# Optimization experiments

Hardware: AMD Instinct MI355X
Metric: run time of the kernel (lower is better)

## Reference

```python
import jax, jax.numpy as jnp
import numpy as np

LN_EPS = 1e-5


def setup_inputs() -> dict:
    key = jax.random.key(0)
    ks = jax.random.split(key, 12)
    B, T, U, H, V = 4, 512, 128, 512, 41
    src = jax.random.normal(ks[0], (B, T, H), dtype=jnp.float32)
    tgt = jax.random.normal(ks[1], (B, U, H), dtype=jnp.float32)
    src_len = jax.random.randint(ks[2], (B,), 1, T + 1, dtype=jnp.int32)
    tgt_len = jax.random.randint(ks[3], (B,), 1, U + 1, dtype=jnp.int32)
    s = 1.0 / np.sqrt(H)
    W1 = jax.random.uniform(ks[4], (H, H), jnp.float32, -s, s)
    b1 = jax.random.uniform(ks[5], (H,), jnp.float32, -s, s)
    W2 = jax.random.uniform(ks[6], (H, H), jnp.float32, -s, s)
    b2 = jax.random.uniform(ks[7], (H,), jnp.float32, -s, s)
    ln_g = jnp.ones((H,), jnp.float32)
    ln_b = jnp.zeros((H,), jnp.float32)
    Wl = jax.random.uniform(ks[8], (H, V), jnp.float32, -s, s)
    bl = jax.random.uniform(ks[9], (V,), jnp.float32, -s, s)
    return dict(source_encodings=src, source_lengths=src_len,
                target_encodings=tgt, target_lengths=tgt_len,
                W1=W1, b1=b1, W2=W2, b2=b2, ln_g=ln_g, ln_b=ln_b,
                Wl=Wl, bl=bl)


def _f_target(tgt, W1, b1, W2, b2, ln_g, ln_b):
    h = jax.nn.gelu(tgt @ W1 + b1, approximate=False)  # exact GELU (torch default)
    h = h @ W2 + b2
    mu = jnp.mean(h, axis=-1, keepdims=True)
    var = jnp.var(h, axis=-1, keepdims=True)
    return (h - mu) * jax.lax.rsqrt(var + LN_EPS) * ln_g + ln_b


def reference(source_encodings, source_lengths, target_encodings, target_lengths,
              W1, b1, W2, b2, ln_g, ln_b, Wl, bl):
    tgt = _f_target(target_encodings, W1, b1, W2, b2, ln_g, ln_b)  # [B,U,H]
    # joint broadcast add: [B,T,1,H] + [B,1,U,H] -> [B,T,U,H]
    joint = source_encodings[:, :, None, :] + tgt[:, None, :, :]
    act = jnp.tanh(joint)
    out = act @ Wl + bl  # [B,T,U,V]
    return out, source_lengths, target_lengths
```

## Files before the change

### kernel.cpp

```cpp
#include <hip/hip_runtime.h>
#include <math.h>

#define Bb 4
#define Tt 512
#define Uu 128
#define Hh 512
#define Vv 41

typedef __attribute__((ext_vector_type(8))) short short8;
typedef __attribute__((ext_vector_type(4))) float f32x4;
typedef __attribute__((ext_vector_type(2))) float v2f;

__device__ __forceinline__ unsigned pack_bf16_rne(float hi, float lo) {
    unsigned xh = __float_as_uint(hi); xh += 0x7fffu + ((xh >> 16) & 1u);
    unsigned xl = __float_as_uint(lo); xl += 0x7fffu + ((xl >> 16) & 1u);
    return __builtin_amdgcn_perm(xh, xl, 0x07060302);
}

__device__ __forceinline__ unsigned short bf16_rne(float v) {
    unsigned x = __float_as_uint(v);
    x += 0x7fffu + ((x >> 16) & 1u);
    return (unsigned short)(x >> 16);
}

__device__ __forceinline__ unsigned tanh2_pack(float x0, float x1) {
    v2f xc;
    xc.x = __builtin_amdgcn_fmed3f(x0, -3.0f, 3.0f);
    xc.y = __builtin_amdgcn_fmed3f(x1, -3.0f, 3.0f);
    v2f t = xc * xc;
    v2f p = t * (v2f){-0.00140725f, -0.00140725f} + (v2f){0.0288922f, 0.0288922f};
    p = p * t + (v2f){-0.2177528f, -0.2177528f};
    p = p * t + (v2f){0.9707868f, 0.9707868f};
    v2f g = xc * p;
    return __builtin_amdgcn_perm(__float_as_uint(g.y), __float_as_uint(g.x), 0x07060302);
}

__global__ __launch_bounds__(256) void prep_pack(
    const float* __restrict__ W1, const float* __restrict__ W2,
    const float* __restrict__ Wl, const float* __restrict__ tgt,
    unsigned short* __restrict__ Wp1, unsigned short* __restrict__ Wp2,
    unsigned short* __restrict__ Wpl, unsigned short* __restrict__ tgtA,
    const int* __restrict__ sl, const int* __restrict__ tl,
    float* __restrict__ lenDst)
{
    __shared__ __align__(16) char smem[16640];
    const int bid = blockIdx.x, tid = threadIdx.x;

    if (bid >= 136) {
        unsigned short (*At)[520] = (unsigned short (*)[520])smem;
        const int rt = bid - 136;
        const float4* t4 = (const float4*)(tgt + (size_t)rt * 16 * Hh);
        #pragma unroll
        for (int j = 0; j < 8; ++j) {
            int fi = j * 256 + tid;
            int row = fi >> 7, c4 = fi & 127;
            float4 v = t4[fi];
            uint2 pk;
            pk.x = pack_bf16_rne(v.y, v.x);
            pk.y = pack_bf16_rne(v.w, v.z);
            *(uint2*)&At[row][c4 * 4] = pk;
        }
        __syncthreads();
        #pragma unroll
        for (int i = 0; i < 4; ++i) {
            int chunk = i * 256 + tid;
            int ks = chunk >> 6, l = chunk & 63;
            int q = l >> 4, nc = l & 15;
            short8 v = *(const short8*)&At[nc][ks * 32 + q * 8];
            *(short8*)(tgtA + ((size_t)(rt * 16 + ks) * 64 + l) * 8) = v;
        }
        return;
    }

    if (bid == 135 && tid < 2 * Bb)
        lenDst[tid] = (tid < Bb) ? (float)sl[tid] : (float)tl[tid - Bb];

    float (*T)[65] = (float (*)[65])smem;
    const float* Wsrc; unsigned short* Wdst; int k0, n0, isWl;
    if (bid < 64)       { Wsrc = W1; Wdst = Wp1; k0 = (bid >> 3) * 64; n0 = (bid & 7) * 64; isWl = 0; }
    else if (bid < 128) { Wsrc = W2; Wdst = Wp2; k0 = ((bid - 64) >> 3) * 64; n0 = ((bid - 64) & 7) * 64; isWl = 0; }
    else                { Wsrc = Wl; Wdst = Wpl; k0 = (bid - 128) * 64; n0 = 0; isWl = 1; }

    #pragma unroll
    for (int i = 0; i < 16; ++i) {
        int idx = i * 256 + tid;
        int kk = idx >> 6, nn = idx & 63;
        float v;
        if (isWl) v = (nn < Vv) ? Wl[(k0 + kk) * Vv + nn] : 0.0f;
        else      v = Wsrc[(size_t)(k0 + kk) * 512 + n0 + nn];
        T[kk][nn] = v;
    }
    __syncthreads();

    #pragma unroll
    for (int i = 0; i < 2; ++i) {
        int task = i * 256 + tid;
        int nn = task & 63, kg = task >> 6;
        if (isWl && nn >= 48) continue;
        int n = n0 + nn, k = k0 + kg * 8;
        float e[8];
        #pragma unroll
        for (int j = 0; j < 8; ++j) e[j] = T[kg * 8 + j][nn];
        uint4 pk;
        pk.x = pack_bf16_rne(e[1], e[0]);
        pk.y = pack_bf16_rne(e[3], e[2]);
        pk.z = pack_bf16_rne(e[5], e[4]);
        pk.w = pack_bf16_rne(e[7], e[6]);
        int ntg = n >> 4, ncol = n & 15;
        int ks = (k >> 5) & 15, quad = (k >> 3) & 3;
        int lane = quad * 16 + ncol;
        *(uint4*)(Wdst + (size_t)((ntg * 16 + ks) * 64 + lane) * 8) = pk;
    }
}

__global__ __launch_bounds__(128) void gemm_t1(
    const unsigned short* __restrict__ tgtA,
    const unsigned short* __restrict__ Wp1, const float* __restrict__ b1,
    unsigned short* __restrict__ h1A)
{
    __shared__ unsigned short At[16][72];
    const int nb = blockIdx.x, rt = blockIdx.y;
    const int tid = threadIdx.x, lane = tid & 63, w = tid >> 6;
    const int ncol = lane & 15, quad = lane >> 4;
    const int nt0 = nb * 4 + w * 2;

    const unsigned short* ap = tgtA + ((size_t)rt * 1024 + lane) * 8;
    const unsigned short* bp = Wp1 + (size_t)lane * 8;

    f32x4 acc0 = (f32x4){0.f,0.f,0.f,0.f}, acc1 = (f32x4){0.f,0.f,0.f,0.f};
    short8 ac  = *(const short8*)(ap);
    short8 b0c = *(const short8*)(bp + (size_t)nt0 * 8192);
    short8 b1c = *(const short8*)(bp + (size_t)(nt0 + 1) * 8192);

    #pragma unroll
    for (int ks = 0; ks < 16; ++ks) {
        short8 an, b0n, b1n;
        if (ks < 15) {
            an  = *(const short8*)(ap + (ks + 1) * 512);
            b0n = *(const short8*)(bp + (size_t)nt0 * 8192 + (ks + 1) * 512);
            b1n = *(const short8*)(bp + (size_t)(nt0 + 1) * 8192 + (ks + 1) * 512);
        }
        acc0 = __builtin_amdgcn_mfma_f32_16x16x32_bf16(ac, b0c, acc0, 0, 0, 0);
        acc1 = __builtin_amdgcn_mfma_f32_16x16x32_bf16(ac, b1c, acc1, 0, 0, 0);
        ac = an; b0c = b0n; b1c = b1n;
    }

    #pragma unroll
    for (int nt = 0; nt < 2; ++nt) {
        int n = nb * 64 + w * 32 + nt * 16 + ncol;
        float bias = b1[n];
        f32x4 A = nt ? acc1 : acc0;
        #pragma unroll
        for (int r = 0; r < 4; ++r) {
            float v = A[r] + bias;
            float g = 0.5f * v * (1.0f + erff(v * 0.70710678118654752f));
            At[quad * 4 + r][w * 32 + nt * 16 + ncol] = bf16_rne(g);
        }
    }
    __syncthreads();

    {
        int g2 = w, l = lane;
        short8 v = *(const short8*)&At[l & 15][g2 * 32 + (l >> 4) * 8];
        int ksg = nb * 2 + g2;
        *(short8*)(h1A + ((size_t)(rt * 16 + ksg) * 64 + l) * 8) = v;
    }
}

__global__ __launch_bounds__(128) void gemm_t2(
    const unsigned short* __restrict__ h1A,
    const unsigned short* __restrict__ Wp2, const float* __restrict__ b2,
    float* __restrict__ h2)
{
    const int nb = blockIdx.x, rt = blockIdx.y;
    const int tid = threadIdx.x, lane = tid & 63, w = tid >> 6;
    const int ncol = lane & 15, quad = lane >> 4;
    const int nt0 = nb * 4 + w * 2;

    const unsigned short* ap = h1A + ((size_t)rt * 1024 + lane) * 8;
    const unsigned short* bp = Wp2 + (size_t)lane * 8;

    f32x4 acc0 = (f32x4){0.f,0.f,0.f,0.f}, acc1 = (f32x4){0.f,0.f,0.f,0.f};
    short8 ac  = *(const short8*)(ap);
    short8 b0c = *(const short8*)(bp + (size_t)nt0 * 8192);
    short8 b1c = *(const short8*)(bp + (size_t)(nt0 + 1) * 8192);

    #pragma unroll
    for (int ks = 0; ks < 16; ++ks) {
        short8 an, b0n, b1n;
        if (ks < 15) {
            an  = *(const short8*)(ap + (ks + 1) * 512);
            b0n = *(const short8*)(bp + (size_t)nt0 * 8192 + (ks + 1) * 512);
            b1n = *(const short8*)(bp + (size_t)(nt0 + 1) * 8192 + (ks + 1) * 512);
        }
        acc0 = __builtin_amdgcn_mfma_f32_16x16x32_bf16(ac, b0c, acc0, 0, 0, 0);
        acc1 = __builtin_amdgcn_mfma_f32_16x16x32_bf16(ac, b1c, acc1, 0, 0, 0);
        ac = an; b0c = b0n; b1c = b1n;
    }

    #pragma unroll
    for (int nt = 0; nt < 2; ++nt) {
        int n = nb * 64 + w * 32 + nt * 16 + ncol;
        float bias = b2[n];
        f32x4 A = nt ? acc1 : acc0;
        #pragma unroll
        for (int r = 0; r < 4; ++r)
            h2[(size_t)(rt * 16 + quad * 4 + r) * 512 + n] = A[r] + bias;
    }
}

__global__ __launch_bounds__(256) void ln_kernel(
    const float* __restrict__ h2, const float* __restrict__ ln_g,
    const float* __restrict__ ln_b, float* __restrict__ tgtPf)
{
    const int r = blockIdx.x * 4 + (threadIdx.x >> 6);
    const int lane = threadIdx.x & 63;
    const float4* row4 = (const float4*)(h2 + (size_t)r * Hh);
    float4 v0 = row4[lane], v1 = row4[lane + 64];
    float s = v0.x + v0.y + v0.z + v0.w + v1.x + v1.y + v1.z + v1.w;
    float q = v0.x*v0.x + v0.y*v0.y + v0.z*v0.z + v0.w*v0.w
            + v1.x*v1.x + v1.y*v1.y + v1.z*v1.z + v1.w*v1.w;
    #pragma unroll
    for (int off = 32; off > 0; off >>= 1) {
        s += __shfl_xor(s, off, 64);
        q += __shfl_xor(q, off, 64);
    }
    float mu = s * (1.0f / Hh);
    float rs = rsqrtf(q * (1.0f / Hh) - mu * mu + 1e-5f);

    float4 g0 = ((const float4*)ln_g)[lane], g1 = ((const float4*)ln_g)[lane + 64];
    float4 be0 = ((const float4*)ln_b)[lane], be1 = ((const float4*)ln_b)[lane + 64];
    float4 o0, o1;
    o0.x = (v0.x - mu) * rs * g0.x + be0.x;  o0.y = (v0.y - mu) * rs * g0.y + be0.y;
    o0.z = (v0.z - mu) * rs * g0.z + be0.z;  o0.w = (v0.w - mu) * rs * g0.w + be0.w;
    o1.x = (v1.x - mu) * rs * g1.x + be1.x;  o1.y = (v1.y - mu) * rs * g1.y + be1.y;
    o1.z = (v1.z - mu) * rs * g1.z + be1.z;  o1.w = (v1.w - mu) * rs * g1.w + be1.w;

    const int bb = r >> 7, u = r & 127;
    float* ob = tgtPf + (size_t)bb * 65536 + u * 8;
    int k0 = lane * 4;
    *(float4*)(ob + (k0 >> 3) * 1024 + (k0 & 7)) = o0;
    int k1 = lane * 4 + 256;
    *(float4*)(ob + (k1 >> 3) * 1024 + (k1 & 7)) = o1;
}

__global__ __launch_bounds__(256) void joint_mfma(
    const float* __restrict__ src, const float* __restrict__ tgtPf,
    const unsigned short* __restrict__ Wpl, const float* __restrict__ bl,
    float* __restrict__ out)
{
    __shared__ float srcl[2 * Hh];

    const int t0 = blockIdx.x * 2, b = blockIdx.y, uh = blockIdx.z;
    const int tid = threadIdx.x;
    const int lane = tid & 63, wave = tid >> 6;
    const int ncol = lane & 15, quad = lane >> 4;

    const float4* s4 = (const float4*)(src + ((size_t)(b * Tt + t0)) * Hh);
    ((float4*)srcl)[tid] = s4[tid];

    const int u0 = uh * 64 + (wave & 1) * 32 + ncol;
    const float* pA = tgtPf + (size_t)b * 65536 + u0 * 8;
    const unsigned short* bp = Wpl + (size_t)lane * 8;

    float4 a0 = *(const float4*)(pA + quad * 1024);
    float4 a1 = *(const float4*)(pA + quad * 1024 + 4);
    float4 c0 = *(const float4*)(pA + quad * 1024 + 128);
    float4 c1 = *(const float4*)(pA + quad * 1024 + 132);
    short8 B0 = *(const short8*)(bp);
    short8 B1 = *(const short8*)(bp + 8192);
    short8 B2 = *(const short8*)(bp + 16384);

    f32x4 acc[2][3];
    #pragma unroll
    for (int nt = 0; nt < 3; ++nt) {
        int n = nt * 16 + ncol;
        float bv = (n < Vv) ? bl[n] : 0.0f;
        acc[0][nt] = (f32x4){bv, bv, bv, bv};
        acc[1][nt] = (f32x4){bv, bv, bv, bv};
    }

    __syncthreads();
    const float* srow = srcl + (wave >> 1) * Hh;
    float4 sA = *(const float4*)(srow + quad * 8);
    float4 sB = *(const float4*)(srow + quad * 8 + 4);

    #pragma unroll 4
    for (int ks = 0; ks < 16; ++ks) {
        float4 na0, na1, nc0, nc1, nsA, nsB;
        short8 nB0, nB1, nB2;
        if (ks < 15) {
            const float* pn = pA + ((ks + 1) * 4 + quad) * 1024;
            na0 = *(const float4*)(pn);
            na1 = *(const float4*)(pn + 4);
            nc0 = *(const float4*)(pn + 128);
            nc1 = *(const float4*)(pn + 132);
            nB0 = *(const short8*)(bp + (ks + 1) * 512);
            nB1 = *(const short8*)(bp + 8192 + (ks + 1) * 512);
            nB2 = *(const short8*)(bp + 16384 + (ks + 1) * 512);
            const float* spn = srow + (ks + 1) * 32 + quad * 8;
            nsA = *(const float4*)(spn);
            nsB = *(const float4*)(spn + 4);
        }

        union { uint4 u; short8 s; } f0, f1;
        f0.u.x = tanh2_pack(sA.x + a0.x, sA.y + a0.y);
        f0.u.y = tanh2_pack(sA.z + a0.z, sA.w + a0.w);
        f0.u.z = tanh2_pack(sB.x + a1.x, sB.y + a1.y);
        f0.u.w = tanh2_pack(sB.z + a1.z, sB.w + a1.w);
        f1.u.x = tanh2_pack(sA.x + c0.x, sA.y + c0.y);
        f1.u.y = tanh2_pack(sA.z + c0.z, sA.w + c0.w);
        f1.u.z = tanh2_pack(sB.x + c1.x, sB.y + c1.y);
        f1.u.w = tanh2_pack(sB.z + c1.z, sB.w + c1.w);

        acc[0][0] = __builtin_amdgcn_mfma_f32_16x16x32_bf16(f0.s, B0, acc[0][0], 0, 0, 0);
        acc[1][0] = __builtin_amdgcn_mfma_f32_16x16x32_bf16(f1.s, B0, acc[1][0], 0, 0, 0);
        acc[0][1] = __builtin_amdgcn_mfma_f32_16x16x32_bf16(f0.s, B1, acc[0][1], 0, 0, 0);
        acc[1][1] = __builtin_amdgcn_mfma_f32_16x16x32_bf16(f1.s, B1, acc[1][1], 0, 0, 0);
        acc[0][2] = __builtin_amdgcn_mfma_f32_16x16x32_bf16(f0.s, B2, acc[0][2], 0, 0, 0);
        acc[1][2] = __builtin_amdgcn_mfma_f32_16x16x32_bf16(f1.s, B2, acc[1][2], 0, 0, 0);

        a0 = na0; a1 = na1; c0 = nc0; c1 = nc1;
        B0 = nB0; B1 = nB1; B2 = nB2;
        sA = nsA; sB = nsB;
    }

    const int t = t0 + (wave >> 1);
    const int ub = uh * 64 + (wave & 1) * 32;
    float* ob = out + ((size_t)(b * Tt + t)) * Uu * Vv;
    #pragma unroll
    for (int mi = 0; mi < 2; ++mi) {
        #pragma unroll
        for (int nt = 0; nt < 3; ++nt) {
            int n = nt * 16 + ncol;
            if (n < Vv) {
                #pragma unroll
                for (int r = 0; r < 4; ++r) {
                    int m = ub + mi * 16 + quad * 4 + r;
                    ob[m * Vv + n] = acc[mi][nt][r];
                }
            }
        }
    }
}

extern "C" void kernel_launch(void* const* d_in, const int* in_sizes, int n_in,
                              void* d_out, int out_size, void* d_ws, size_t ws_size,
                              hipStream_t stream)
{
    const float* src  = (const float*)d_in[0];
    const int*   slen = (const int*)  d_in[1];
    const float* tgt  = (const float*)d_in[2];
    const int*   tlen = (const int*)  d_in[3];
    const float* W1   = (const float*)d_in[4];
    const float* b1   = (const float*)d_in[5];
    const float* W2   = (const float*)d_in[6];
    const float* b2   = (const float*)d_in[7];
    const float* ln_g = (const float*)d_in[8];
    const float* ln_b = (const float*)d_in[9];
    const float* Wl   = (const float*)d_in[10];
    const float* bl   = (const float*)d_in[11];

    float* out = (float*)d_out;
    char* ws = (char*)d_ws;
    float*          tgtPf = (float*)(ws);
    unsigned short* Wp1   = (unsigned short*)(ws + 1048576);
    unsigned short* Wp2   = (unsigned short*)(ws + 1572864);
    unsigned short* Wpl   = (unsigned short*)(ws + 2097152);
    unsigned short* tgtA  = (unsigned short*)(ws + 2162688);
    unsigned short* h1A   = (unsigned short*)(ws + 2686976);
    float*          h2    = (float*)(ws + 3211264);

    hipLaunchKernelGGL(prep_pack, dim3(168), dim3(256), 0, stream,
                       W1, W2, Wl, tgt, Wp1, Wp2, Wpl, tgtA,
                       slen, tlen, out + (size_t)Bb * Tt * Uu * Vv);
    hipLaunchKernelGGL(gemm_t1, dim3(8, 32), dim3(128), 0, stream,
                       tgtA, Wp1, b1, h1A);
    hipLaunchKernelGGL(gemm_t2, dim3(8, 32), dim3(128), 0, stream,
                       h1A, Wp2, b2, h2);
    hipLaunchKernelGGL(ln_kernel, dim3(128), dim3(256), 0, stream,
                       h2, ln_g, ln_b, tgtPf);
    hipLaunchKernelGGL(joint_mfma, dim3(Tt / 2, Bb, 2), dim3(256), 0, stream,
                       src, tgtPf, Wpl, bl, out);
}
```

Baseline: 141.5 us.

## Fuse second GEMM with LayerNorm, store target in bf16, double-buffer joint loads

Merges gemm_t2 and the LayerNorm kernel into one 512-thread kernel per 16-row tile. Each block computes full rows into shared memory, normalizes them and writes the target projection as packed bf16 instead of fp32. The joint kernel reads the bf16 target, which halves that load traffic, and prefetches A/B fragments two steps ahead with a fully unrolled loop. The cost is only 32 blocks for the second GEMM, higher register pressure in the joint kernel, and an extra bf16 rounding of the target activations.

```diff
diff --git a/kernel.cpp b/kernel.cpp
--- a/kernel.cpp
+++ b/kernel.cpp
@@ -22,6 +22,9 @@
     x += 0x7fffu + ((x >> 16) & 1u);
     return (unsigned short)(x >> 16);
 }
+
+__device__ __forceinline__ float bf16lo(unsigned u) { return __uint_as_float(u << 16); }
+__device__ __forceinline__ float bf16hi(unsigned u) { return __uint_as_float(u & 0xffff0000u); }
 
 __device__ __forceinline__ unsigned tanh2_pack(float x0, float x1) {
     v2f xc;
@@ -160,92 +163,104 @@
     __syncthreads();
 
     {
-        int g2 = w, l = lane;
-        short8 v = *(const short8*)&At[l & 15][g2 * 32 + (l >> 4) * 8];
-        int ksg = nb * 2 + g2;
+        int l = lane;
+        short8 v = *(const short8*)&At[l & 15][w * 32 + (l >> 4) * 8];
+        int ksg = nb * 2 + w;
         *(short8*)(h1A + ((size_t)(rt * 16 + ksg) * 64 + l) * 8) = v;
     }
 }
 
-__global__ __launch_bounds__(128) void gemm_t2(
+__global__ __launch_bounds__(512) void gemm_t2ln(
     const unsigned short* __restrict__ h1A,
     const unsigned short* __restrict__ Wp2, const float* __restrict__ b2,
-    float* __restrict__ h2)
+    const float* __restrict__ ln_g, const float* __restrict__ ln_b,
+    unsigned short* __restrict__ tgtPb)
 {
-    const int nb = blockIdx.x, rt = blockIdx.y;
+    __shared__ float Ct[16][520];
+    const int rt = blockIdx.x;
     const int tid = threadIdx.x, lane = tid & 63, w = tid >> 6;
     const int ncol = lane & 15, quad = lane >> 4;
-    const int nt0 = nb * 4 + w * 2;
+    const int nt0 = w * 4;
 
     const unsigned short* ap = h1A + ((size_t)rt * 1024 + lane) * 8;
-    const unsigned short* bp = Wp2 + (size_t)lane * 8;
-
-    f32x4 acc0 = (f32x4){0.f,0.f,0.f,0.f}, acc1 = (f32x4){0.f,0.f,0.f,0.f};
-    short8 ac  = *(const short8*)(ap);
-    short8 b0c = *(const short8*)(bp + (size_t)nt0 * 8192);
-    short8 b1c = *(const short8*)(bp + (size_t)(nt0 + 1) * 8192);
+    const unsigned short* bp = Wp2 + (size_t)lane * 8 + (size_t)nt0 * 8192;
+
+    f32x4 acc[4];
+    #pragma unroll
+    for (int i = 0; i < 4; ++i) acc[i] = (f32x4){0.f, 0.f, 0.f, 0.f};
+
+    short8 ac = *(const short8*)(ap);
+    short8 bc[4];
+    #pragma unroll
+    for (int i = 0; i < 4; ++i) bc[i] = *(const short8*)(bp + (size_t)i * 8192);
 
     #pragma unroll
     for (int ks = 0; ks < 16; ++ks) {
-        short8 an, b0n, b1n;
+        short8 an, bn[4];
         if (ks < 15) {
-            an  = *(const short8*)(ap + (ks + 1) * 512);
-            b0n = *(const short8*)(bp + (size_t)nt0 * 8192 + (ks + 1) * 512);
-            b1n = *(const short8*)(bp + (size_t)(nt0 + 1) * 8192 + (ks + 1) * 512);
-        }
-        acc0 = __builtin_amdgcn_mfma_f32_16x16x32_bf16(ac, b0c, acc0, 0, 0, 0);
-        acc1 = __builtin_amdgcn_mfma_f32_16x16x32_bf16(ac, b1c, acc1, 0, 0, 0);
-        ac = an; b0c = b0n; b1c = b1n;
-    }
-
-    #pragma unroll
-    for (int nt = 0; nt < 2; ++nt) {
-        int n = nb * 64 + w * 32 + nt * 16 + ncol;
+            an = *(const short8*)(ap + (ks + 1) * 512);
+            #pragma unroll
+            for (int i = 0; i < 4; ++i)
+                bn[i] = *(const short8*)(bp + (size_t)i * 8192 + (ks + 1) * 512);
+        }
+        #pragma unroll
+        for (int i = 0; i < 4; ++i)
+            acc[i] = __builtin_amdgcn_mfma_f32_16x16x32_bf16(ac, bc[i], acc[i], 0, 0, 0);
+        ac = an;
+        #pragma unroll
+        for (int i = 0; i < 4; ++i) bc[i] = bn[i];
+    }
+
+    #pragma unroll
+    for (int nt = 0; nt < 4; ++nt) {
+        int n = w * 64 + nt * 16 + ncol;
         float bias = b2[n];
-        f32x4 A = nt ? acc1 : acc0;
         #pragma unroll
         for (int r = 0; r < 4; ++r)
-            h2[(size_t)(rt * 16 + quad * 4 + r) * 512 + n] = A[r] + bias;
-    }
-}
-
-__global__ __launch_bounds__(256) void ln_kernel(
-    const float* __restrict__ h2, const float* __restrict__ ln_g,
-    const float* __restrict__ ln_b, float* __restrict__ tgtPf)
-{
-    const int r = blockIdx.x * 4 + (threadIdx.x >> 6);
-    const int lane = threadIdx.x & 63;
-    const float4* row4 = (const float4*)(h2 + (size_t)r * Hh);
-    float4 v0 = row4[lane], v1 = row4[lane + 64];
-    float s = v0.x + v0.y + v0.z + v0.w + v1.x + v1.y + v1.z + v1.w;
-    float q = v0.x*v0.x + v0.y*v0.y + v0.z*v0.z + v0.w*v0.w
-            + v1.x*v1.x + v1.y*v1.y + v1.z*v1.z + v1.w*v1.w;
-    #pragma unroll
-    for (int off = 32; off > 0; off >>= 1) {
-        s += __shfl_xor(s, off, 64);
-        q += __shfl_xor(q, off, 64);
-    }
-    float mu = s * (1.0f / Hh);
-    float rs = rsqrtf(q * (1.0f / Hh) - mu * mu + 1e-5f);
-
-    float4 g0 = ((const float4*)ln_g)[lane], g1 = ((const float4*)ln_g)[lane + 64];
-    float4 be0 = ((const float4*)ln_b)[lane], be1 = ((const float4*)ln_b)[lane + 64];
-    float4 o0, o1;
-    o0.x = (v0.x - mu) * rs * g0.x + be0.x;  o0.y = (v0.y - mu) * rs * g0.y + be0.y;
-    o0.z = (v0.z - mu) * rs * g0.z + be0.z;  o0.w = (v0.w - mu) * rs * g0.w + be0.w;
-    o1.x = (v1.x - mu) * rs * g1.x + be1.x;  o1.y = (v1.y - mu) * rs * g1.y + be1.y;
-    o1.z = (v1.z - mu) * rs * g1.z + be1.z;  o1.w = (v1.w - mu) * rs * g1.w + be1.w;
-
-    const int bb = r >> 7, u = r & 127;
-    float* ob = tgtPf + (size_t)bb * 65536 + u * 8;
-    int k0 = lane * 4;
-    *(float4*)(ob + (k0 >> 3) * 1024 + (k0 & 7)) = o0;
-    int k1 = lane * 4 + 256;
-    *(float4*)(ob + (k1 >> 3) * 1024 + (k1 & 7)) = o1;
+            Ct[quad * 4 + r][n] = acc[nt][r] + bias;
+    }
+    __syncthreads();
+
+    #pragma unroll
+    for (int rr = 0; rr < 2; ++rr) {
+        const int row = w * 2 + rr;
+        const float4* cr = (const float4*)&Ct[row][0];
+        float4 v0 = cr[lane], v1 = cr[lane + 64];
+        float s = v0.x + v0.y + v0.z + v0.w + v1.x + v1.y + v1.z + v1.w;
+        float q = v0.x*v0.x + v0.y*v0.y + v0.z*v0.z + v0.w*v0.w
+                + v1.x*v1.x + v1.y*v1.y + v1.z*v1.z + v1.w*v1.w;
+        #pragma unroll
+        for (int off = 32; off > 0; off >>= 1) {
+            s += __shfl_xor(s, off, 64);
+            q += __shfl_xor(q, off, 64);
+        }
+        float mu = s * (1.0f / Hh);
+        float rs = rsqrtf(q * (1.0f / Hh) - mu * mu + 1e-5f);
+
+        const int r = rt * 16 + row;
+        const int bb = r >> 7, u = r & 127;
+        #pragma unroll
+        for (int j = 0; j < 2; ++j) {
+            int k0 = j * 256 + lane * 4;
+            float4 v = j ? v1 : v0;
+            float4 g4 = ((const float4*)ln_g)[j * 64 + lane];
+            float4 b4 = ((const float4*)ln_b)[j * 64 + lane];
+            float4 o;
+            o.x = (v.x - mu) * rs * g4.x + b4.x;
+            o.y = (v.y - mu) * rs * g4.y + b4.y;
+            o.z = (v.z - mu) * rs * g4.z + b4.z;
+            o.w = (v.w - mu) * rs * g4.w + b4.w;
+            uint2 pk;
+            pk.x = pack_bf16_rne(o.y, o.x);
+            pk.y = pack_bf16_rne(o.w, o.z);
+            int chunk = k0 >> 3, half = (k0 >> 2) & 1;
+            *(uint2*)(tgtPb + ((size_t)(bb * 64 + chunk) * 128 + u) * 8 + half * 4) = pk;
+        }
+    }
 }
 
 __global__ __launch_bounds__(256) void joint_mfma(
-    const float* __restrict__ src, const float* __restrict__ tgtPf,
+    const float* __restrict__ src, const unsigned short* __restrict__ tgtPb,
     const unsigned short* __restrict__ Wpl, const float* __restrict__ bl,
     float* __restrict__ out)
 {
@@ -260,16 +275,25 @@
     ((float4*)srcl)[tid] = s4[tid];
 
     const int u0 = uh * 64 + (wave & 1) * 32 + ncol;
-    const float* pA = tgtPf + (size_t)b * 65536 + u0 * 8;
+    const unsigned short* pA = tgtPb + (size_t)b * 65536;
     const unsigned short* bp = Wpl + (size_t)lane * 8;
 
-    float4 a0 = *(const float4*)(pA + quad * 1024);
-    float4 a1 = *(const float4*)(pA + quad * 1024 + 4);
-    float4 c0 = *(const float4*)(pA + quad * 1024 + 128);
-    float4 c1 = *(const float4*)(pA + quad * 1024 + 132);
-    short8 B0 = *(const short8*)(bp);
-    short8 B1 = *(const short8*)(bp + 8192);
-    short8 B2 = *(const short8*)(bp + 16384);
+    uint4 Aa[2], Ac[2];
+    short8 Bq[2][3];
+    {
+        const unsigned short* p0 = pA + ((size_t)(0 * 4 + quad) * 128) * 8;
+        Aa[0] = *(const uint4*)(p0 + u0 * 8);
+        Ac[0] = *(const uint4*)(p0 + (u0 + 16) * 8);
+        Bq[0][0] = *(const short8*)(bp);
+        Bq[0][1] = *(const short8*)(bp + 8192);
+        Bq[0][2] = *(const short8*)(bp + 16384);
+        const unsigned short* p1 = pA + ((size_t)(1 * 4 + quad) * 128) * 8;
+        Aa[1] = *(const uint4*)(p1 + u0 * 8);
+        Ac[1] = *(const uint4*)(p1 + (u0 + 16) * 8);
+        Bq[1][0] = *(const short8*)(bp + 512);
+        Bq[1][1] = *(const short8*)(bp + 8192 + 512);
+        Bq[1][2] = *(const short8*)(bp + 16384 + 512);
+    }
 
     f32x4 acc[2][3];
     #pragma unroll
@@ -285,33 +309,35 @@
     float4 sA = *(const float4*)(srow + quad * 8);
     float4 sB = *(const float4*)(srow + quad * 8 + 4);
 
-    #pragma unroll 4
+    #pragma unroll
     for (int ks = 0; ks < 16; ++ks) {
-        float4 na0, na1, nc0, nc1, nsA, nsB;
-        short8 nB0, nB1, nB2;
+        const int st = ks & 1;
+        uint4 a = Aa[st], c = Ac[st];
+        short8 B0 = Bq[st][0], B1 = Bq[st][1], B2 = Bq[st][2];
+
+        if (ks + 2 < 16) {
+            const unsigned short* pn = pA + ((size_t)((ks + 2) * 4 + quad) * 128) * 8;
+            Aa[st] = *(const uint4*)(pn + u0 * 8);
+            Ac[st] = *(const uint4*)(pn + (u0 + 16) * 8);
+            Bq[st][0] = *(const short8*)(bp + (ks + 2) * 512);
+            Bq[st][1] = *(const short8*)(bp + 8192 + (ks + 2) * 512);
+            Bq[st][2] = *(const short8*)(bp + 16384 + (ks + 2) * 512);
+        }
+        float4 nsA, nsB;
         if (ks < 15) {
-            const float* pn = pA + ((ks + 1) * 4 + quad) * 1024;
-            na0 = *(const float4*)(pn);
-            na1 = *(const float4*)(pn + 4);
-            nc0 = *(const float4*)(pn + 128);
-            nc1 = *(const float4*)(pn + 132);
-            nB0 = *(const short8*)(bp + (ks + 1) * 512);
-            nB1 = *(const short8*)(bp + 8192 + (ks + 1) * 512);
-            nB2 = *(const short8*)(bp + 16384 + (ks + 1) * 512);
-            const float* spn = srow + (ks + 1) * 32 + quad * 8;
-            nsA = *(const float4*)(spn);
-            nsB = *(const float4*)(spn + 4);
+            nsA = *(const float4*)(srow + (ks + 1) * 32 + quad * 8);
+            nsB = *(const float4*)(srow + (ks + 1) * 32 + quad * 8 + 4);
         }
 
         union { uint4 u; short8 s; } f0, f1;
-        f0.u.x = tanh2_pack(sA.x + a0.x, sA.y + a0.y);
-        f0.u.y = tanh2_pack(sA.z + a0.z, sA.w + a0.w);
-        f0.u.z = tanh2_pack(sB.x + a1.x, sB.y + a1.y);
-        f0.u.w = tanh2_pack(sB.z + a1.z, sB.w + a1.w);
-        f1.u.x = tanh2_pack(sA.x + c0.x, sA.y + c0.y);
-        f1.u.y = tanh2_pack(sA.z + c0.z, sA.w + c0.w);
-        f1.u.z = tanh2_pack(sB.x + c1.x, sB.y + c1.y);
-        f1.u.w = tanh2_pack(sB.z + c1.z, sB.w + c1.w);
+        f0.u.x = tanh2_pack(sA.x + bf16lo(a.x), sA.y + bf16hi(a.x));
+        f0.u.y = tanh2_pack(sA.z + bf16lo(a.y), sA.w + bf16hi(a.y));
+        f0.u.z = tanh2_pack(sB.x + bf16lo(a.z), sB.y + bf16hi(a.z));
+        f0.u.w = tanh2_pack(sB.z + bf16lo(a.w), sB.w + bf16hi(a.w));
+        f1.u.x = tanh2_pack(sA.x + bf16lo(c.x), sA.y + bf16hi(c.x));
+        f1.u.y = tanh2_pack(sA.z + bf16lo(c.y), sA.w + bf16hi(c.y));
+        f1.u.z = tanh2_pack(sB.x + bf16lo(c.z), sB.y + bf16hi(c.z));
+        f1.u.w = tanh2_pack(sB.z + bf16lo(c.w), sB.w + bf16hi(c.w));
 
         acc[0][0] = __builtin_amdgcn_mfma_f32_16x16x32_bf16(f0.s, B0, acc[0][0], 0, 0, 0);
         acc[1][0] = __builtin_amdgcn_mfma_f32_16x16x32_bf16(f1.s, B0, acc[1][0], 0, 0, 0);
@@ -320,8 +346,6 @@
         acc[0][2] = __builtin_amdgcn_mfma_f32_16x16x32_bf16(f0.s, B2, acc[0][2], 0, 0, 0);
         acc[1][2] = __builtin_amdgcn_mfma_f32_16x16x32_bf16(f1.s, B2, acc[1][2], 0, 0, 0);
 
-        a0 = na0; a1 = na1; c0 = nc0; c1 = nc1;
-        B0 = nB0; B1 = nB1; B2 = nB2;
         sA = nsA; sB = nsB;
     }
 
@@ -363,23 +387,20 @@
 
     float* out = (float*)d_out;
     char* ws = (char*)d_ws;
-    float*          tgtPf = (float*)(ws);
-    unsigned short* Wp1   = (unsigned short*)(ws + 1048576);
-    unsigned short* Wp2   = (unsigned short*)(ws + 1572864);
-    unsigned short* Wpl   = (unsigned short*)(ws + 2097152);
-    unsigned short* tgtA  = (unsigned short*)(ws + 2162688);
-    unsigned short* h1A   = (unsigned short*)(ws + 2686976);
-    float*          h2    = (float*)(ws + 3211264);
+    unsigned short* tgtPb = (unsigned short*)(ws);
+    unsigned short* Wp1   = (unsigned short*)(ws + 524288);
+    unsigned short* Wp2   = (unsigned short*)(ws + 1048576);
+    unsigned short* Wpl   = (unsigned short*)(ws + 1572864);
+    unsigned short* tgtA  = (unsigned short*)(ws + 1638400);
+    unsigned short* h1A   = (unsigned short*)(ws + 2162688);
 
     hipLaunchKernelGGL(prep_pack, dim3(168), dim3(256), 0, stream,
                        W1, W2, Wl, tgt, Wp1, Wp2, Wpl, tgtA,
                        slen, tlen, out + (size_t)Bb * Tt * Uu * Vv);
     hipLaunchKernelGGL(gemm_t1, dim3(8, 32), dim3(128), 0, stream,
                        tgtA, Wp1, b1, h1A);
-    hipLaunchKernelGGL(gemm_t2, dim3(8, 32), dim3(128), 0, stream,
-                       h1A, Wp2, b2, h2);
-    hipLaunchKernelGGL(ln_kernel, dim3(128), dim3(256), 0, stream,
-                       h2, ln_g, ln_b, tgtPf);
+    hipLaunchKernelGGL(gemm_t2ln, dim3(32), dim3(512), 0, stream,
+                       h1A, Wp2, b2, ln_g, ln_b, tgtPb);
     hipLaunchKernelGGL(joint_mfma, dim3(Tt / 2, Bb, 2), dim3(256), 0, stream,
-                       src, tgtPf, Wpl, bl, out);
-}
+                       src, tgtPb, Wpl, bl, out);
+}
```

Result: no change. 142.9 us (+0.9%).
